# Performance work log

Hardware: AMD Instinct MI355X
Metric: run time of the kernel (lower is better)

Reference implementation:

```python
import jax, jax.numpy as jnp
import numpy as np

D_LOW = 32
LAGS = [1, 2, 4, 8]
# Upper-triangular pair indices (offset=1), matching torch.triu_indices(d_low, d_low, 1)
IDX_I, IDX_J = np.triu_indices(D_LOW, k=1)
IDX_I = jnp.asarray(IDX_I)
IDX_J = jnp.asarray(IDX_J)
EPS = 1e-6


def setup_inputs() -> dict:
    key = jax.random.key(0)
    ks = jax.random.split(key, 7)
    b, n, d_model = 4, 4096, 1024
    d_plucker = D_LOW * (D_LOW - 1) // 2  # 496
    s = lambda fan_in: 1.0 / np.sqrt(fan_in)
    return {
        "x": jax.random.normal(ks[0], (b, n, d_model), dtype=jnp.float32),
        "W_red": jax.random.normal(ks[1], (d_model, D_LOW), dtype=jnp.float32) * s(d_model),
        "b_red": jax.random.normal(ks[2], (D_LOW,), dtype=jnp.float32) * s(d_model),
        "W_exp": jax.random.normal(ks[3], (d_plucker, d_model), dtype=jnp.float32) * s(d_plucker),
        "b_exp": jax.random.normal(ks[4], (d_model,), dtype=jnp.float32) * s(d_plucker),
        "W_gate": jax.random.normal(ks[5], (2 * d_model, d_model), dtype=jnp.float32) * s(2 * d_model),
        "b_gate": jax.random.normal(ks[6], (d_model,), dtype=jnp.float32) * s(2 * d_model),
    }


def reference(x, W_red, b_red, W_exp, b_exp, W_gate, b_gate):
    b, n, _ = x.shape
    d_plucker = D_LOW * (D_LOW - 1) // 2
    z = x @ W_red + b_red  # [b, n, d_low]
    plucker_total = jnp.zeros((b, n, d_plucker), dtype=x.dtype)
    counts = jnp.zeros((b, n, 1), dtype=x.dtype)
    for lag in LAGS:
        if lag <= 0 or lag >= n:
            continue
        z_curr = z[:, lag:, :]   # [b, n-lag, d_low]
        z_past = z[:, :-lag, :]  # [b, n-lag, d_low]
        # Antisymmetric Plucker coordinates over upper-triangular index pairs
        p = (z_curr[:, :, IDX_I] * z_past[:, :, IDX_J]
             - z_curr[:, :, IDX_J] * z_past[:, :, IDX_I])  # [b, n-lag, d_plucker]
        norm = jnp.linalg.norm(p, axis=-1, keepdims=True)
        p = p / jnp.maximum(norm, EPS)
        plucker_total = plucker_total.at[:, lag:, :].add(p)
        counts = counts.at[:, lag:, :].add(1.0)
    counts = jnp.maximum(counts, 1.0)
    plucker_avg = plucker_total / counts
    g_avg = plucker_avg @ W_exp + b_exp  # [b, n, d_model]
    concat = jnp.concatenate([x, g_avg], axis=-1)  # [b, n, 2*d_model]
    gate = jax.nn.sigmoid(concat @ W_gate + b_gate)
    return gate * x + (1.0 - gate) * g_avg
```

## Files before the change

### kernel.cpp

```cpp
#include <hip/hip_runtime.h>
#include <hip/hip_bf16.h>
#include <math.h>

#define B_DIM   4
#define N_DIM   4096
#define D_MODEL 1024
#define D_LOW   32
#define NPAIR   496
#define NROWS   (B_DIM * N_DIM)
#define KPAD3   512
#define LDA2    1536

typedef __bf16 bf16;
typedef __bf16 bf16x8 __attribute__((ext_vector_type(8)));
typedef __bf16 bf16x4 __attribute__((ext_vector_type(4)));
typedef float  f32x4  __attribute__((ext_vector_type(4)));

#define GLOAD_LDS16(g, l) __builtin_amdgcn_global_load_lds( \
    (__attribute__((address_space(1))) void*)(g),           \
    (__attribute__((address_space(3))) void*)(l), 16, 0, 0)

__global__ __launch_bounds__(256) void wred_t(const float* __restrict__ Wr,
                                              bf16* __restrict__ WrT) {
    __shared__ float tile[32][33];
    const int t  = threadIdx.x;
    const int kb = blockIdx.x * 32;
    {
        int k = t >> 3, c4 = (t & 7) * 4;
        float4 v = *reinterpret_cast<const float4*>(&Wr[(size_t)(kb + k) * 32 + c4]);
        tile[k][c4 + 0] = v.x; tile[k][c4 + 1] = v.y;
        tile[k][c4 + 2] = v.z; tile[k][c4 + 3] = v.w;
    }
    __syncthreads();
    {
        int c = t >> 3, kq = (t & 7) * 4;
        bf16x4 o = { (bf16)tile[kq + 0][c], (bf16)tile[kq + 1][c],
                     (bf16)tile[kq + 2][c], (bf16)tile[kq + 3][c] };
        *reinterpret_cast<bf16x4*>(&WrT[(size_t)c * 1024 + kb + kq]) = o;
    }
}

__global__ __launch_bounds__(256) void k1_mfma(const float* __restrict__ x,
                                               const bf16* __restrict__ WrT,
                                               bf16* __restrict__ a2,
                                               float* __restrict__ zpart) {
    const int t    = threadIdx.x;
    const int wv   = t >> 6, lane = t & 63;
    const int l15  = lane & 15, lhi = lane >> 4;
    const int kc   = blockIdx.x;
    const int mt   = blockIdx.y;
    const int row  = mt * 64 + wv * 16 + l15;
    const int kb   = kc * 512;

    f32x4 accz[2] = { (f32x4){0.f,0.f,0.f,0.f}, (f32x4){0.f,0.f,0.f,0.f} };

#pragma unroll
    for (int ks = 0; ks < 16; ++ks) {
        const int k0 = kb + ks * 32 + lhi * 8;
        const float4 u0 = *reinterpret_cast<const float4*>(&x[(size_t)row * 1024 + k0]);
        const float4 u1 = *reinterpret_cast<const float4*>(&x[(size_t)row * 1024 + k0 + 4]);
        bf16x8 af = { (bf16)u0.x, (bf16)u0.y, (bf16)u0.z, (bf16)u0.w,
                      (bf16)u1.x, (bf16)u1.y, (bf16)u1.z, (bf16)u1.w };
        *reinterpret_cast<bf16x8*>(&a2[(size_t)row * LDA2 + k0]) = af;
        const bf16x8 b0 = *reinterpret_cast<const bf16x8*>(
            &WrT[(size_t)l15 * 1024 + kb + ks * 32 + lhi * 8]);
        const bf16x8 b1 = *reinterpret_cast<const bf16x8*>(
            &WrT[(size_t)(16 + l15) * 1024 + kb + ks * 32 + lhi * 8]);
        accz[0] = __builtin_amdgcn_mfma_f32_16x16x32_bf16(af, b0, accz[0], 0, 0, 0);
        accz[1] = __builtin_amdgcn_mfma_f32_16x16x32_bf16(af, b1, accz[1], 0, 0, 0);
    }
#pragma unroll
    for (int cg = 0; cg < 2; ++cg)
#pragma unroll
        for (int r = 0; r < 4; ++r) {
            const int rout = mt * 64 + wv * 16 + lhi * 4 + r;
            zpart[((size_t)kc * NROWS + rout) * 32 + cg * 16 + l15] = accz[cg][r];
        }
}

__global__ __launch_bounds__(256) void k2_plucker(const float* __restrict__ zpart,
                                                  const float* __restrict__ br,
                                                  bf16* __restrict__ a2) {
    const int wv   = threadIdx.x >> 6;
    const int lane = threadIdx.x & 63;
    const int row  = blockIdx.x * 4 + wv;
    const int t    = row & (N_DIM - 1);
    const int c    = lane & 31;
    const float bias = br[c];

    float zc = bias;
#pragma unroll
    for (int p = 0; p < 2; ++p)
        zc += zpart[((size_t)p * NROWS + row) * 32 + c];

    float zp[4];
    float red[9];
    red[0] = zc * zc;
#pragma unroll
    for (int li = 0; li < 4; ++li) {
        const int lag = 1 << li;
        float v = 0.f;
        if (t >= lag) {
            v = bias;
#pragma unroll
            for (int p = 0; p < 2; ++p)
                v += zpart[((size_t)p * NROWS + (row - lag)) * 32 + c];
        }
        zp[li] = v;
        red[1 + li] = zc * zp[li];
        red[5 + li] = zp[li] * zp[li];
    }
#pragma unroll
    for (int m = 1; m < 32; m <<= 1) {
#pragma unroll
        for (int i = 0; i < 9; ++i) red[i] += __shfl_xor(red[i], m);
    }
    float cnt = 0.f;
#pragma unroll
    for (int li = 0; li < 4; ++li) cnt += (t >= (1 << li)) ? 1.f : 0.f;
    const float inv = 1.f / fmaxf(cnt, 1.f);

    float w = 0.f;
#pragma unroll
    for (int li = 0; li < 4; ++li) {
        float n2 = fmaxf(red[0] * red[5 + li] - red[1 + li] * red[1 + li], 0.f);
        float nr = sqrtf(n2);
        float s  = (t >= (1 << li)) ? inv / fmaxf(nr, 1e-6f) : 0.f;
        w += s * zp[li];
    }

#pragma unroll
    for (int u = 0; u < 8; ++u) {
        const int k = u * 64 + lane;
        float v = 0.f;
        if (k < NPAIR) {
            int kk = k, i = 0;
            while (kk >= 31 - i) { kk -= 31 - i; ++i; }
            const int j = i + 1 + kk;
            float zci = __shfl(zc, i), zcj = __shfl(zc, j);
            float wi  = __shfl(w, i),  wj  = __shfl(w, j);
            v = zci * wj - zcj * wi;
        }
        a2[(size_t)row * LDA2 + 1024 + k] = (bf16)v;
    }
}

__global__ __launch_bounds__(256) void transpose_cvt(const float* __restrict__ src,
                                                     bf16* __restrict__ dst,
                                                     int Ksrc, int Kpad) {
    __shared__ float tile[32][36];
    const int t  = threadIdx.x;
    const int kb = blockIdx.x * 32;
    const int nb = blockIdx.y * 32;
    int li = t * 4;
    int kl = li >> 5, nl = li & 31;
    float4 v = {0.f, 0.f, 0.f, 0.f};
    if (kb + kl < Ksrc)
        v = *reinterpret_cast<const float4*>(&src[(size_t)(kb + kl) * 1024 + nb + nl]);
    tile[kl][nl + 0] = v.x; tile[kl][nl + 1] = v.y;
    tile[kl][nl + 2] = v.z; tile[kl][nl + 3] = v.w;
    __syncthreads();
    int nl2 = li >> 5, kl2 = li & 31;
    bf16x4 o = { (bf16)tile[kl2 + 0][nl2], (bf16)tile[kl2 + 1][nl2],
                 (bf16)tile[kl2 + 2][nl2], (bf16)tile[kl2 + 3][nl2] };
    *reinterpret_cast<bf16x4*>(&dst[(size_t)(nb + nl2) * Kpad + kb + kl2]) = o;
}

__global__ __launch_bounds__(256) void we_cvt_be(const float* __restrict__ We,
                                                 const float* __restrict__ be,
                                                 bf16* __restrict__ WeB) {
    size_t o = ((size_t)blockIdx.x * 256 + threadIdx.x) * 4;
    int row = (int)(o >> 10), col = (int)(o & 1023);
    float4 v = {0.f, 0.f, 0.f, 0.f};
    if (row < NPAIR)      v = *reinterpret_cast<const float4*>(&We[(size_t)row * 1024 + col]);
    else if (row == NPAIR) v = *reinterpret_cast<const float4*>(&be[col]);
    bf16x4 b = { (bf16)v.x, (bf16)v.y, (bf16)v.z, (bf16)v.w };
    *reinterpret_cast<bf16x4*>(&WeB[o]) = b;
}

__global__ __launch_bounds__(256) void wcomb_mfma(const bf16* __restrict__ A,
                                                  const bf16* __restrict__ Bt,
                                                  bf16* __restrict__ BcT) {
    __shared__ bf16 As[128 * 32];
    __shared__ bf16 Bs[128 * 32];
    const int t    = threadIdx.x;
    const int mb   = blockIdx.y * 128;
    const int nbq  = blockIdx.x * 128;
    const int w    = t >> 6, lane = t & 63;
    const int wr   = w >> 1, wc = w & 1;
    const int l15  = lane & 15, lhi = lane >> 4;

    f32x4 acc[4][4];
#pragma unroll
    for (int mt = 0; mt < 4; ++mt)
#pragma unroll
        for (int nt = 0; nt < 4; ++nt) acc[mt][nt] = (f32x4){0.f, 0.f, 0.f, 0.f};

    const int li0 = t, li1 = t + 256;
    const int r0 = li0 >> 2, c0 = (li0 & 3) * 8;
    const int r1 = li1 >> 2, c1 = (li1 & 3) * 8;

    for (int kb = 0; kb < 1024; kb += 32) {
        GLOAD_LDS16(A  + (size_t)(mb + r0) * 1024 + kb + c0, As + li0 * 8);
        GLOAD_LDS16(A  + (size_t)(mb + r1) * 1024 + kb + c1, As + li1 * 8);
        GLOAD_LDS16(Bt + (size_t)(nbq + r0) * 1024 + kb + c0, Bs + li0 * 8);
        GLOAD_LDS16(Bt + (size_t)(nbq + r1) * 1024 + kb + c1, Bs + li1 * 8);
        __syncthreads();
        bf16x8 a[4], b[4];
#pragma unroll
        for (int mt = 0; mt < 4; ++mt)
            a[mt] = *reinterpret_cast<const bf16x8*>(
                As + (wr * 64 + mt * 16 + l15) * 32 + lhi * 8);
#pragma unroll
        for (int nt = 0; nt < 4; ++nt)
            b[nt] = *reinterpret_cast<const bf16x8*>(
                Bs + (wc * 64 + nt * 16 + l15) * 32 + lhi * 8);
#pragma unroll
        for (int mt = 0; mt < 4; ++mt)
#pragma unroll
            for (int nt = 0; nt < 4; ++nt)
                acc[mt][nt] = __builtin_amdgcn_mfma_f32_16x16x32_bf16(
                    a[mt], b[nt], acc[mt][nt], 0, 0, 0);
        __syncthreads();
    }
#pragma unroll
    for (int mt = 0; mt < 4; ++mt)
#pragma unroll
        for (int nt = 0; nt < 4; ++nt) {
            const int col = nbq + wc * 64 + nt * 16 + l15;
#pragma unroll
            for (int r = 0; r < 4; ++r) {
                const int row = mb + wr * 64 + mt * 16 + lhi * 4 + r;
                BcT[(size_t)row * 1536 + 1024 + col] = (bf16)acc[mt][nt][r];
            }
        }
}

__global__ __launch_bounds__(256) void bgc_extract(const float* __restrict__ bg,
                                                   const bf16* __restrict__ BcT,
                                                   float* __restrict__ bgc) {
    int n = blockIdx.x * 256 + threadIdx.x;
    bgc[n] = bg[n] + (float)BcT[(size_t)n * 1536 + 1024 + NPAIR];
}

template <int KDIM, int LDAp, int LDBp, bool GATE>
__global__ __launch_bounds__(512, 2) void gemm2b(const bf16* __restrict__ A,
                                                 const bf16* __restrict__ Bt,
                                                 const float* __restrict__ bias,
                                                 const bf16* __restrict__ gsrc,
                                                 bf16* __restrict__ gdst,
                                                 float* __restrict__ out) {
    extern __shared__ char lds[];
    const int t    = threadIdx.x;
    const int w    = t >> 6, lane = t & 63;
    const int wr   = w >> 2, wc = w & 3;
    const int l15  = lane & 15, lhi = lane >> 4;

    const int fid = blockIdx.x;
    const int xcd = fid & 7, loc = fid >> 3;
    const int mb  = (xcd * 8 + (loc >> 2)) * 256;
    const int nb  = (loc & 3) * 256;

    const int srow = t >> 3;
    const int scol = ((t & 7) ^ (srow & 7)) * 8;
    const size_t aOff = (size_t)(mb + srow) * LDAp + scol;
    const size_t bOff = (size_t)(nb + srow) * LDBp + scol;
    char* const ldsA = lds;
    char* const ldsB = lds + 65536;

#define STAGE_A(d, h, kb) do { \
    GLOAD_LDS16(A + aOff + (size_t)((h) * 128) * LDAp + (kb),      ldsA + (d) * 32768 + (h) * 16384 + t * 16); \
    GLOAD_LDS16(A + aOff + (size_t)((h) * 128 + 64) * LDAp + (kb), ldsA + (d) * 32768 + (h) * 16384 + 8192 + t * 16); } while (0)
#define STAGE_B(d, h, kb) do { \
    GLOAD_LDS16(Bt + bOff + (size_t)((h) * 128) * LDBp + (kb),      ldsB + (d) * 32768 + (h) * 16384 + t * 16); \
    GLOAD_LDS16(Bt + bOff + (size_t)((h) * 128 + 64) * LDBp + (kb), ldsB + (d) * 32768 + (h) * 16384 + 8192 + t * 16); } while (0)

    const int swx = (l15 & 7) << 4;
#define LDAF(d, mq_) do { const char* Ab_ = ldsA + (d) * 32768 + wr * 16384; \
    _Pragma("unroll") for (int mf = 0; mf < 4; ++mf) \
    _Pragma("unroll") for (int ks = 0; ks < 2; ++ks) { \
        int lin = ((mq_) * 64 + mf * 16 + l15) * 128 + ks * 64 + lhi * 16; \
        afr[mf][ks] = *reinterpret_cast<const bf16x8*>(Ab_ + (lin ^ swx)); } } while (0)
#define LDBF(d, nq_) do { const char* Bb_ = ldsB + (d) * 32768 + (wc >> 1) * 16384; \
    _Pragma("unroll") for (int nf = 0; nf < 2; ++nf) \
    _Pragma("unroll") for (int ks = 0; ks < 2; ++ks) { \
        int lin = ((wc & 1) * 64 + (nq_) * 32 + nf * 16 + l15) * 128 + ks * 64 + lhi * 16; \
        bfr[nf][ks] = *reinterpret_cast<const bf16x8*>(Bb_ + (lin ^ swx)); } } while (0)
#define MMA(mq_, nq_) do { __builtin_amdgcn_s_setprio(1); \
    _Pragma("unroll") for (int mf = 0; mf < 4; ++mf) \
    _Pragma("unroll") for (int nf = 0; nf < 2; ++nf) \
    _Pragma("unroll") for (int ks = 0; ks < 2; ++ks) \
        acc[(mq_) * 4 + mf][(nq_) * 2 + nf] = __builtin_amdgcn_mfma_f32_16x16x32_bf16( \
            afr[mf][ks], bfr[nf][ks], acc[(mq_) * 4 + mf][(nq_) * 2 + nf], 0, 0, 0); \
    __builtin_amdgcn_s_setprio(0); } while (0)
#define BAR() asm volatile("s_barrier" ::: "memory")

    f32x4 acc[8][4];
#pragma unroll
    for (int i = 0; i < 8; ++i)
#pragma unroll
        for (int j = 0; j < 4; ++j) acc[i][j] = (f32x4){0.f, 0.f, 0.f, 0.f};
    bf16x8 afr[4][2], bfr[2][2];

    STAGE_A(0, 0, 0); STAGE_A(0, 1, 0);
    STAGE_B(0, 0, 0); STAGE_B(0, 1, 0);

    const int NT = KDIM / 64;
    for (int kt = 0; kt < NT; ++kt) {
        const int d  = kt & 1;
        const int kn = (kt + 1) * 64;
        const bool pre = (kt + 1 < NT);

        BAR();
        if (pre) {
            STAGE_A(d ^ 1, 0, kn); STAGE_A(d ^ 1, 1, kn);
            STAGE_B(d ^ 1, 0, kn); STAGE_B(d ^ 1, 1, kn);
            asm volatile("s_waitcnt vmcnt(8)" ::: "memory");
        } else {
            asm volatile("s_waitcnt vmcnt(0)" ::: "memory");
        }
        BAR();

        LDAF(d, 0); LDBF(d, 0);
        MMA(0, 0);
        LDAF(d, 1);
        MMA(1, 0);
        LDBF(d, 1);
        MMA(1, 1);
        LDAF(d, 0);
        MMA(0, 1);
    }
#undef STAGE_A
#undef STAGE_B
#undef LDAF
#undef LDBF
#undef MMA
#undef BAR

#pragma unroll
    for (int mi = 0; mi < 8; ++mi) {
#pragma unroll
        for (int nf = 0; nf < 4; ++nf) {
            const int col = nb + wc * 64 + nf * 16 + l15;
            const float bv = bias[col];
#pragma unroll
            for (int r = 0; r < 4; ++r) {
                const int row = mb + wr * 128 + mi * 16 + lhi * 4 + r;
                float v = acc[mi][nf][r] + bv;
                if constexpr (GATE) {
                    float gate = 1.f / (1.f + expf(-v));
                    float xv = (float)A[(size_t)row * LDAp + col];
                    float gv = (float)gsrc[(size_t)row * D_MODEL + col];
                    out[(size_t)row * D_MODEL + col] = gate * xv + (1.f - gate) * gv;
                } else {
                    gdst[(size_t)row * D_MODEL + col] = (bf16)v;
                }
            }
        }
    }
}

extern "C" void kernel_launch(void* const* d_in, const int* in_sizes, int n_in,
                              void* d_out, int out_size, void* d_ws, size_t ws_size,
                              hipStream_t stream) {
    const float* x  = (const float*)d_in[0];
    const float* Wr = (const float*)d_in[1];
    const float* br = (const float*)d_in[2];
    const float* We = (const float*)d_in[3];
    const float* be = (const float*)d_in[4];
    const float* Wg = (const float*)d_in[5];
    const float* bg = (const float*)d_in[6];
    float* out = (float*)d_out;

    char* ws = (char*)d_ws;
    bf16*  gbuf  = (bf16*)(ws);
    float* zpart = (float*)(ws);
    bf16*  A2    = (bf16*)(ws + (32u << 20));
    bf16*  WeT   = (bf16*)(ws + (80u << 20));
    bf16*  BcT   = (bf16*)(ws + (81u << 20));
    bf16*  WgbT  = (bf16*)(ws + (84u << 20));
    bf16*  WeB   = (bf16*)(ws + (86u << 20));
    float* bgc   = (float*)(ws + (87u << 20));
    bf16*  WrT   = (bf16*)(ws + (88u << 20));

    (void)hipFuncSetAttribute(reinterpret_cast<const void*>(&gemm2b<KPAD3, LDA2, KPAD3, false>),
                              hipFuncAttributeMaxDynamicSharedMemorySize, 131072);
    (void)hipFuncSetAttribute(reinterpret_cast<const void*>(&gemm2b<1536, LDA2, 1536, true>),
                              hipFuncAttributeMaxDynamicSharedMemorySize, 131072);

    wred_t<<<32, 256, 0, stream>>>(Wr, WrT);
    k1_mfma<<<dim3(2, 256), 256, 0, stream>>>(x, WrT, A2, zpart);
    k2_plucker<<<NROWS / 4, 256, 0, stream>>>(zpart, br, A2);

    transpose_cvt<<<dim3(KPAD3 / 32, 1024 / 32), 256, 0, stream>>>(We, WeT, NPAIR, KPAD3);
    transpose_cvt<<<dim3(1024 / 32, 1024 / 32), 256, 0, stream>>>(Wg, BcT, 1024, 1536);
    transpose_cvt<<<dim3(1024 / 32, 1024 / 32), 256, 0, stream>>>(Wg + (size_t)1024 * 1024, WgbT, 1024, 1024);
    we_cvt_be<<<512, 256, 0, stream>>>(We, be, WeB);
    wcomb_mfma<<<dim3(4, 8), 256, 0, stream>>>(WgbT, WeB, BcT);
    bgc_extract<<<4, 256, 0, stream>>>(bg, BcT, bgc);

    gemm2b<KPAD3, LDA2, KPAD3, false><<<256, 512, 131072, stream>>>(
        A2 + 1024, WeT, be, nullptr, gbuf, nullptr);
    gemm2b<1536, LDA2, 1536, true><<<256, 512, 131072, stream>>>(
        A2, BcT, bgc, gbuf, nullptr, out);
}
```

Before: 169.4 us.

## Restructure GEMM main loop with two-deep prefetch and interleaved staged loads

```diff
diff --git a/kernel.cpp b/kernel.cpp
--- a/kernel.cpp
+++ b/kernel.cpp
@@ -244,7 +244,7 @@
 }
 
 template <int KDIM, int LDAp, int LDBp, bool GATE>
-__global__ __launch_bounds__(512, 2) void gemm2b(const bf16* __restrict__ A,
+__global__ __launch_bounds__(512, 2) void gemmzr(const bf16* __restrict__ A,
                                                  const bf16* __restrict__ Bt,
                                                  const float* __restrict__ bias,
                                                  const bf16* __restrict__ gsrc,
@@ -281,17 +281,17 @@
     _Pragma("unroll") for (int ks = 0; ks < 2; ++ks) { \
         int lin = ((mq_) * 64 + mf * 16 + l15) * 128 + ks * 64 + lhi * 16; \
         afr[mf][ks] = *reinterpret_cast<const bf16x8*>(Ab_ + (lin ^ swx)); } } while (0)
-#define LDBF(d, nq_) do { const char* Bb_ = ldsB + (d) * 32768 + (wc >> 1) * 16384; \
+#define LDBF(dst, d, nq_) do { const char* Bb_ = ldsB + (d) * 32768 + (wc >> 1) * 16384; \
     _Pragma("unroll") for (int nf = 0; nf < 2; ++nf) \
     _Pragma("unroll") for (int ks = 0; ks < 2; ++ks) { \
         int lin = ((wc & 1) * 64 + (nq_) * 32 + nf * 16 + l15) * 128 + ks * 64 + lhi * 16; \
-        bfr[nf][ks] = *reinterpret_cast<const bf16x8*>(Bb_ + (lin ^ swx)); } } while (0)
-#define MMA(mq_, nq_) do { __builtin_amdgcn_s_setprio(1); \
+        dst[nf][ks] = *reinterpret_cast<const bf16x8*>(Bb_ + (lin ^ swx)); } } while (0)
+#define MMA(bset, mq_, nq_) do { __builtin_amdgcn_s_setprio(1); \
     _Pragma("unroll") for (int mf = 0; mf < 4; ++mf) \
     _Pragma("unroll") for (int nf = 0; nf < 2; ++nf) \
     _Pragma("unroll") for (int ks = 0; ks < 2; ++ks) \
         acc[(mq_) * 4 + mf][(nq_) * 2 + nf] = __builtin_amdgcn_mfma_f32_16x16x32_bf16( \
-            afr[mf][ks], bfr[nf][ks], acc[(mq_) * 4 + mf][(nq_) * 2 + nf], 0, 0, 0); \
+            afr[mf][ks], bset[nf][ks], acc[(mq_) * 4 + mf][(nq_) * 2 + nf], 0, 0, 0); \
     __builtin_amdgcn_s_setprio(0); } while (0)
 #define BAR() asm volatile("s_barrier" ::: "memory")
 
@@ -300,35 +300,49 @@
     for (int i = 0; i < 8; ++i)
 #pragma unroll
         for (int j = 0; j < 4; ++j) acc[i][j] = (f32x4){0.f, 0.f, 0.f, 0.f};
-    bf16x8 afr[4][2], bfr[2][2];
-
-    STAGE_A(0, 0, 0); STAGE_A(0, 1, 0);
-    STAGE_B(0, 0, 0); STAGE_B(0, 1, 0);
-
-    const int NT = KDIM / 64;
-    for (int kt = 0; kt < NT; ++kt) {
-        const int d  = kt & 1;
-        const int kn = (kt + 1) * 64;
-        const bool pre = (kt + 1 < NT);
-
-        BAR();
-        if (pre) {
-            STAGE_A(d ^ 1, 0, kn); STAGE_A(d ^ 1, 1, kn);
-            STAGE_B(d ^ 1, 0, kn); STAGE_B(d ^ 1, 1, kn);
-            asm volatile("s_waitcnt vmcnt(8)" ::: "memory");
-        } else {
-            asm volatile("s_waitcnt vmcnt(0)" ::: "memory");
-        }
-        BAR();
-
-        LDAF(d, 0); LDBF(d, 0);
-        MMA(0, 0);
-        LDAF(d, 1);
-        MMA(1, 0);
-        LDBF(d, 1);
-        MMA(1, 1);
-        LDAF(d, 0);
-        MMA(0, 1);
+    bf16x8 afr[4][2], bfr0[2][2], bfrB[2][2];
+
+    STAGE_A(0, 0, 0);  STAGE_A(0, 1, 0);  STAGE_B(0, 0, 0);  STAGE_B(0, 1, 0);
+    STAGE_A(1, 0, 64); STAGE_A(1, 1, 64); STAGE_B(1, 0, 64); STAGE_B(1, 1, 64);
+
+    const int NT    = KDIM / 64;
+    const int ITERS = NT / 2;
+    for (int it = 0; it < ITERS; ++it) {
+        const int kA = (it * 2 + 2) * 64;
+        const int kB = (it * 2 + 3) * 64;
+        const bool p2 = (it * 2 + 2) < NT;
+        const bool p3 = (it * 2 + 3) < NT;
+
+        asm volatile("s_waitcnt vmcnt(8)" ::: "memory");
+        BAR();
+        LDAF(0, 0); LDBF(bfr0, 0, 0);
+        MMA(bfr0, 0, 0);
+        BAR();
+        LDBF(bfrB, 0, 1);
+        MMA(bfrB, 0, 1);
+        BAR();
+        if (p2) { STAGE_B(0, 0, kA); STAGE_B(0, 1, kA); }
+        LDAF(0, 1);
+        MMA(bfrB, 1, 1);
+        BAR();
+        if (p2) { STAGE_A(0, 0, kA); STAGE_A(0, 1, kA); }
+        MMA(bfr0, 1, 0);
+
+        if (p2) asm volatile("s_waitcnt vmcnt(8)" ::: "memory");
+        else    asm volatile("s_waitcnt vmcnt(0)" ::: "memory");
+        BAR();
+        LDAF(1, 0); LDBF(bfr0, 1, 0);
+        MMA(bfr0, 0, 0);
+        BAR();
+        LDBF(bfrB, 1, 1);
+        MMA(bfrB, 0, 1);
+        BAR();
+        if (p3) { STAGE_B(1, 0, kB); STAGE_B(1, 1, kB); }
+        LDAF(1, 1);
+        MMA(bfrB, 1, 1);
+        BAR();
+        if (p3) { STAGE_A(1, 0, kB); STAGE_A(1, 1, kB); }
+        MMA(bfr0, 1, 0);
     }
 #undef STAGE_A
 #undef STAGE_B
@@ -383,9 +397,9 @@
     float* bgc   = (float*)(ws + (87u << 20));
     bf16*  WrT   = (bf16*)(ws + (88u << 20));
 
-    (void)hipFuncSetAttribute(reinterpret_cast<const void*>(&gemm2b<KPAD3, LDA2, KPAD3, false>),
+    (void)hipFuncSetAttribute(reinterpret_cast<const void*>(&gemmzr<KPAD3, LDA2, KPAD3, false>),
                               hipFuncAttributeMaxDynamicSharedMemorySize, 131072);
-    (void)hipFuncSetAttribute(reinterpret_cast<const void*>(&gemm2b<1536, LDA2, 1536, true>),
+    (void)hipFuncSetAttribute(reinterpret_cast<const void*>(&gemmzr<1536, LDA2, 1536, true>),
                               hipFuncAttributeMaxDynamicSharedMemorySize, 131072);
 
     wred_t<<<32, 256, 0, stream>>>(Wr, WrT);
@@ -399,8 +413,8 @@
     wcomb_mfma<<<dim3(4, 8), 256, 0, stream>>>(WgbT, WeB, BcT);
     bgc_extract<<<4, 256, 0, stream>>>(bg, BcT, bgc);
 
-    gemm2b<KPAD3, LDA2, KPAD3, false><<<256, 512, 131072, stream>>>(
+    gemmzr<KPAD3, LDA2, KPAD3, false><<<256, 512, 131072, stream>>>(
         A2 + 1024, WeT, be, nullptr, gbuf, nullptr);
-    gemm2b<1536, LDA2, 1536, true><<<256, 512, 131072, stream>>>(
+    gemmzr<1536, LDA2, 1536, true><<<256, 512, 131072, stream>>>(
         A2, BcT, bgc, gbuf, nullptr, out);
 }
```

After: 164.6 us. 2.9% less time.

## Replace double-buffered 256x256 GEMM with single-buffered 256x128 tile kernel

Applied to the files above, without the earlier changes.

```diff
diff --git a/kernel.cpp b/kernel.cpp
--- a/kernel.cpp
+++ b/kernel.cpp
@@ -244,7 +244,7 @@
 }
 
 template <int KDIM, int LDAp, int LDBp, bool GATE>
-__global__ __launch_bounds__(512, 2) void gemm2b(const bf16* __restrict__ A,
+__global__ __launch_bounds__(512, 2) void gemm97(const bf16* __restrict__ A,
                                                  const bf16* __restrict__ Bt,
                                                  const float* __restrict__ bias,
                                                  const bf16* __restrict__ gsrc,
@@ -253,100 +253,81 @@
     extern __shared__ char lds[];
     const int t    = threadIdx.x;
     const int w    = t >> 6, lane = t & 63;
-    const int wr   = w >> 2, wc = w & 3;
+    const int wr   = w >> 1, wc = w & 1;
     const int l15  = lane & 15, lhi = lane >> 4;
 
     const int fid = blockIdx.x;
     const int xcd = fid & 7, loc = fid >> 3;
-    const int mb  = (xcd * 8 + (loc >> 2)) * 256;
-    const int nb  = (loc & 3) * 256;
+    const int mb  = (xcd * 8 + (loc >> 3)) * 256;
+    const int nb  = (loc & 7) * 128;
 
     const int srow = t >> 3;
     const int scol = ((t & 7) ^ (srow & 7)) * 8;
     const size_t aOff = (size_t)(mb + srow) * LDAp + scol;
     const size_t bOff = (size_t)(nb + srow) * LDBp + scol;
     char* const ldsA = lds;
-    char* const ldsB = lds + 65536;
-
-#define STAGE_A(d, h, kb) do { \
-    GLOAD_LDS16(A + aOff + (size_t)((h) * 128) * LDAp + (kb),      ldsA + (d) * 32768 + (h) * 16384 + t * 16); \
-    GLOAD_LDS16(A + aOff + (size_t)((h) * 128 + 64) * LDAp + (kb), ldsA + (d) * 32768 + (h) * 16384 + 8192 + t * 16); } while (0)
-#define STAGE_B(d, h, kb) do { \
-    GLOAD_LDS16(Bt + bOff + (size_t)((h) * 128) * LDBp + (kb),      ldsB + (d) * 32768 + (h) * 16384 + t * 16); \
-    GLOAD_LDS16(Bt + bOff + (size_t)((h) * 128 + 64) * LDBp + (kb), ldsB + (d) * 32768 + (h) * 16384 + 8192 + t * 16); } while (0)
+    char* const ldsB = lds + 32768;
 
     const int swx = (l15 & 7) << 4;
-#define LDAF(d, mq_) do { const char* Ab_ = ldsA + (d) * 32768 + wr * 16384; \
-    _Pragma("unroll") for (int mf = 0; mf < 4; ++mf) \
-    _Pragma("unroll") for (int ks = 0; ks < 2; ++ks) { \
-        int lin = ((mq_) * 64 + mf * 16 + l15) * 128 + ks * 64 + lhi * 16; \
-        afr[mf][ks] = *reinterpret_cast<const bf16x8*>(Ab_ + (lin ^ swx)); } } while (0)
-#define LDBF(d, nq_) do { const char* Bb_ = ldsB + (d) * 32768 + (wc >> 1) * 16384; \
-    _Pragma("unroll") for (int nf = 0; nf < 2; ++nf) \
-    _Pragma("unroll") for (int ks = 0; ks < 2; ++ks) { \
-        int lin = ((wc & 1) * 64 + (nq_) * 32 + nf * 16 + l15) * 128 + ks * 64 + lhi * 16; \
-        bfr[nf][ks] = *reinterpret_cast<const bf16x8*>(Bb_ + (lin ^ swx)); } } while (0)
-#define MMA(mq_, nq_) do { __builtin_amdgcn_s_setprio(1); \
-    _Pragma("unroll") for (int mf = 0; mf < 4; ++mf) \
-    _Pragma("unroll") for (int nf = 0; nf < 2; ++nf) \
-    _Pragma("unroll") for (int ks = 0; ks < 2; ++ks) \
-        acc[(mq_) * 4 + mf][(nq_) * 2 + nf] = __builtin_amdgcn_mfma_f32_16x16x32_bf16( \
-            afr[mf][ks], bfr[nf][ks], acc[(mq_) * 4 + mf][(nq_) * 2 + nf], 0, 0, 0); \
-    __builtin_amdgcn_s_setprio(0); } while (0)
-#define BAR() asm volatile("s_barrier" ::: "memory")
-
-    f32x4 acc[8][4];
-#pragma unroll
-    for (int i = 0; i < 8; ++i)
+
+    f32x4 acc[4][4];
+#pragma unroll
+    for (int i = 0; i < 4; ++i)
 #pragma unroll
         for (int j = 0; j < 4; ++j) acc[i][j] = (f32x4){0.f, 0.f, 0.f, 0.f};
-    bf16x8 afr[4][2], bfr[2][2];
-
-    STAGE_A(0, 0, 0); STAGE_A(0, 1, 0);
-    STAGE_B(0, 0, 0); STAGE_B(0, 1, 0);
+    bf16x8 afr[4][2], bfr[4][2];
 
     const int NT = KDIM / 64;
     for (int kt = 0; kt < NT; ++kt) {
-        const int d  = kt & 1;
-        const int kn = (kt + 1) * 64;
-        const bool pre = (kt + 1 < NT);
-
-        BAR();
-        if (pre) {
-            STAGE_A(d ^ 1, 0, kn); STAGE_A(d ^ 1, 1, kn);
-            STAGE_B(d ^ 1, 0, kn); STAGE_B(d ^ 1, 1, kn);
-            asm volatile("s_waitcnt vmcnt(8)" ::: "memory");
-        } else {
-            asm volatile("s_waitcnt vmcnt(0)" ::: "memory");
-        }
-        BAR();
-
-        LDAF(d, 0); LDBF(d, 0);
-        MMA(0, 0);
-        LDAF(d, 1);
-        MMA(1, 0);
-        LDBF(d, 1);
-        MMA(1, 1);
-        LDAF(d, 0);
-        MMA(0, 1);
-    }
-#undef STAGE_A
-#undef STAGE_B
-#undef LDAF
-#undef LDBF
-#undef MMA
-#undef BAR
-
-#pragma unroll
-    for (int mi = 0; mi < 8; ++mi) {
+        const int kb = kt * 64;
+        __builtin_amdgcn_s_barrier();
+#pragma unroll
+        for (int q = 0; q < 4; ++q)
+            GLOAD_LDS16(A + aOff + (size_t)(q * 64) * LDAp + kb,
+                        ldsA + q * 8192 + t * 16);
+#pragma unroll
+        for (int q = 0; q < 2; ++q)
+            GLOAD_LDS16(Bt + bOff + (size_t)(q * 64) * LDBp + kb,
+                        ldsB + q * 8192 + t * 16);
+        asm volatile("s_waitcnt vmcnt(0)" ::: "memory");
+        __builtin_amdgcn_s_barrier();
+
+#pragma unroll
+        for (int mf = 0; mf < 4; ++mf)
+#pragma unroll
+            for (int ks = 0; ks < 2; ++ks) {
+                int lin = (wr * 64 + mf * 16 + l15) * 128 + ks * 64 + lhi * 16;
+                afr[mf][ks] = *reinterpret_cast<const bf16x8*>(ldsA + (lin ^ swx));
+            }
+#pragma unroll
+        for (int nf = 0; nf < 4; ++nf)
+#pragma unroll
+            for (int ks = 0; ks < 2; ++ks) {
+                int lin = (wc * 64 + nf * 16 + l15) * 128 + ks * 64 + lhi * 16;
+                bfr[nf][ks] = *reinterpret_cast<const bf16x8*>(ldsB + (lin ^ swx));
+            }
+        __builtin_amdgcn_s_setprio(1);
+#pragma unroll
+        for (int mf = 0; mf < 4; ++mf)
+#pragma unroll
+            for (int nf = 0; nf < 4; ++nf)
+#pragma unroll
+                for (int ks = 0; ks < 2; ++ks)
+                    acc[mf][nf] = __builtin_amdgcn_mfma_f32_16x16x32_bf16(
+                        afr[mf][ks], bfr[nf][ks], acc[mf][nf], 0, 0, 0);
+        __builtin_amdgcn_s_setprio(0);
+    }
+
+#pragma unroll
+    for (int mf = 0; mf < 4; ++mf) {
 #pragma unroll
         for (int nf = 0; nf < 4; ++nf) {
             const int col = nb + wc * 64 + nf * 16 + l15;
             const float bv = bias[col];
 #pragma unroll
             for (int r = 0; r < 4; ++r) {
-                const int row = mb + wr * 128 + mi * 16 + lhi * 4 + r;
-                float v = acc[mi][nf][r] + bv;
+                const int row = mb + wr * 64 + mf * 16 + lhi * 4 + r;
+                float v = acc[mf][nf][r] + bv;
                 if constexpr (GATE) {
                     float gate = 1.f / (1.f + expf(-v));
                     float xv = (float)A[(size_t)row * LDAp + col];
@@ -383,10 +364,10 @@
     float* bgc   = (float*)(ws + (87u << 20));
     bf16*  WrT   = (bf16*)(ws + (88u << 20));
 
-    (void)hipFuncSetAttribute(reinterpret_cast<const void*>(&gemm2b<KPAD3, LDA2, KPAD3, false>),
-                              hipFuncAttributeMaxDynamicSharedMemorySize, 131072);
-    (void)hipFuncSetAttribute(reinterpret_cast<const void*>(&gemm2b<1536, LDA2, 1536, true>),
-                              hipFuncAttributeMaxDynamicSharedMemorySize, 131072);
+    (void)hipFuncSetAttribute(reinterpret_cast<const void*>(&gemm97<KPAD3, LDA2, KPAD3, false>),
+                              hipFuncAttributeMaxDynamicSharedMemorySize, 49152);
+    (void)hipFuncSetAttribute(reinterpret_cast<const void*>(&gemm97<1536, LDA2, 1536, true>),
+                              hipFuncAttributeMaxDynamicSharedMemorySize, 49152);
 
     wred_t<<<32, 256, 0, stream>>>(Wr, WrT);
     k1_mfma<<<dim3(2, 256), 256, 0, stream>>>(x, WrT, A2, zpart);
@@ -399,8 +380,8 @@
     wcomb_mfma<<<dim3(4, 8), 256, 0, stream>>>(WgbT, WeB, BcT);
     bgc_extract<<<4, 256, 0, stream>>>(bg, BcT, bgc);
 
-    gemm2b<KPAD3, LDA2, KPAD3, false><<<256, 512, 131072, stream>>>(
+    gemm97<KPAD3, LDA2, KPAD3, false><<<512, 512, 49152, stream>>>(
         A2 + 1024, WeT, be, nullptr, gbuf, nullptr);
-    gemm2b<1536, LDA2, 1536, true><<<256, 512, 131072, stream>>>(
+    gemm97<1536, LDA2, 1536, true><<<512, 512, 49152, stream>>>(
         A2, BcT, bgc, gbuf, nullptr, out);
 }
```

Measured after the change: 197.7 us. 1.17x slower.
